# Performance work log

Hardware: AMD Instinct MI355X
Metric: run time of the kernel (lower is better)

Reference implementation:

```python
import jax, jax.numpy as jnp
import numpy as np

D_MODEL = 1024
NUM_HEADS = 16


def setup_inputs() -> dict:
    key = jax.random.key(0)
    ks = jax.random.split(key, 5)
    x = jax.random.normal(ks[0], (1, 4096, D_MODEL), dtype=jnp.float32)
    # Linear stores weight as [out_features, in_features]; init ~ trunc_normal, scaled for stability
    scale = 0.02
    wq = jax.random.normal(ks[1], (D_MODEL, D_MODEL), dtype=jnp.float32) * scale
    wk = jax.random.normal(ks[2], (D_MODEL, D_MODEL), dtype=jnp.float32) * scale
    wv = jax.random.normal(ks[3], (D_MODEL, D_MODEL), dtype=jnp.float32) * scale
    wo = jax.random.normal(ks[4], (D_MODEL, D_MODEL), dtype=jnp.float32) * scale
    return {"x": x, "wq": wq, "wk": wk, "wv": wv, "wo": wo}


def reference(x, wq, wk, wv, wo):
    # x: [B, S, D]; weights: [D, D] stored as [out, in] (y = x @ W.T)
    B, S, D = x.shape
    H = NUM_HEADS
    d_k = D // H
    q = x @ wq.T  # [B, S, D]
    k = x @ wk.T
    v = x @ wv.T
    # torch.split along last dim == reshape into contiguous head chunks
    qh = q.reshape(B, S, H, d_k).transpose(0, 2, 1, 3)  # [B, H, S, d_k]
    kh = k.reshape(B, S, H, d_k).transpose(0, 2, 1, 3)
    vh = v.reshape(B, S, H, d_k).transpose(0, 2, 1, 3)
    scores = jnp.einsum("bhqd,bhkd->bhqk", qh, kh) / jnp.sqrt(jnp.asarray(d_k, x.dtype))
    causal = jnp.tril(jnp.ones((S, S), dtype=bool))
    # original uses masked_fill(mask == 0, -10000.0), not -inf
    scores = jnp.where(causal, scores, jnp.asarray(-10000.0, x.dtype))
    attn = jax.nn.softmax(scores, axis=-1)  # stable (subtracts max), same math as module's Softmax
    ctx = jnp.einsum("bhqk,bhkd->bhqd", attn, vh)  # [B, H, S, d_k]
    ctx = ctx.transpose(0, 2, 1, 3).reshape(B, S, D)  # concat heads along last dim
    return ctx @ wo.T
```

## Files before the change

kernel.cpp:

```cpp
#include <hip/hip_runtime.h>
#include <stdint.h>

typedef short s16x8 __attribute__((ext_vector_type(8)));
typedef short s16x4 __attribute__((ext_vector_type(4)));
typedef float f32x4 __attribute__((ext_vector_type(4)));
typedef unsigned short u16;

#define S_LEN 4096
#define DM    1024
#define NH    16

__device__ __forceinline__ u16 f2bf(float f) {
  unsigned int u; __builtin_memcpy(&u, &f, 4);
  return (u16)((u + 0x7fffu + ((u >> 16) & 1u)) >> 16);
}

__device__ __forceinline__ void glds16(const void* gsrc, void* lds_uniform) {
  __builtin_amdgcn_global_load_lds(
      (const __attribute__((address_space(1))) unsigned int*)gsrc,
      (__attribute__((address_space(3))) unsigned int*)(unsigned int)(uintptr_t)lds_uniform,
      16, 0, 0);
}

__global__ __launch_bounds__(256)
void cast_all(const float* __restrict__ x,  const float* __restrict__ wq,
              const float* __restrict__ wk, const float* __restrict__ wv,
              const float* __restrict__ wo,
              u16* __restrict__ xb,  u16* __restrict__ wqb, u16* __restrict__ wkb,
              u16* __restrict__ wvb, u16* __restrict__ wob) {
  const int i = blockIdx.x * 256 + threadIdx.x;
  const float* src; u16* dst; int off;
  if (i < (1 << 20)) { src = x; dst = xb; off = i; }
  else {
    const int j = i - (1 << 20);
    const int seg = j >> 18;
    off = j & ((1 << 18) - 1);
    if (seg == 0)      { src = wq; dst = wqb; }
    else if (seg == 1) { src = wk; dst = wkb; }
    else if (seg == 2) { src = wv; dst = wvb; }
    else               { src = wo; dst = wob; }
  }
  float4 v = ((const float4*)src)[off];
  ushort4 o;
  o.x = f2bf(v.x); o.y = f2bf(v.y); o.z = f2bf(v.z); o.w = f2bf(v.w);
  ((ushort4*)dst)[off] = o;
}

#define GEMM_PROLOGUE()                                                        \
  __shared__ u16 SM[32768];                                                    \
  const int tid  = threadIdx.x;                                                \
  const int lane = tid & 63;                                                   \
  const int wave = tid >> 6;                                                   \
  const int g    = lane >> 4;                                                  \
  const int lr   = lane & 15;                                                  \
  const int x7   = lane & 7;                                                   \
  const int wr   = wave >> 1;                                                  \
  const int wc   = wave & 1;                                                   \
  const int a_base = wr * 8192 + lr * 128 + ((g ^ x7) << 4);                   \
  const int b_base = 0x8000 + wc * 8192 + lr * 128 + ((g ^ x7) << 4);          \
  const int stg_row = wave * 8 + (lane >> 3);                                  \
  const int gc      = (lane & 7) ^ (lane >> 3);                                \
  const int stg_dst = wave * 1024;                                             \
  const f32x4 zz = {0.f, 0.f, 0.f, 0.f};                                       \
  f32x4 acc[4][4];                                                             \
  _Pragma("unroll") for (int i = 0; i < 4; ++i)                                \
      _Pragma("unroll") for (int j = 0; j < 4; ++j) acc[i][j] = zz;

#define GEMM_KLOOP(Aptr, Wptr)                                                 \
  const u16* pa0 = Aptr + (size_t)(m0 +  0 + stg_row) * 1024 + gc * 8;         \
  const u16* pa1 = Aptr + (size_t)(m0 + 32 + stg_row) * 1024 + gc * 8;         \
  const u16* pa2 = Aptr + (size_t)(m0 + 64 + stg_row) * 1024 + gc * 8;         \
  const u16* pa3 = Aptr + (size_t)(m0 + 96 + stg_row) * 1024 + gc * 8;         \
  const u16* pw0 = Wptr + (size_t)(n0 +  0 + stg_row) * 1024 + gc * 8;         \
  const u16* pw1 = Wptr + (size_t)(n0 + 32 + stg_row) * 1024 + gc * 8;         \
  const u16* pw2 = Wptr + (size_t)(n0 + 64 + stg_row) * 1024 + gc * 8;         \
  const u16* pw3 = Wptr + (size_t)(n0 + 96 + stg_row) * 1024 + gc * 8;         \
  {                                                                            \
    glds16(pa0, (char*)SM + stg_dst);                                          \
    glds16(pa1, (char*)SM + 4096  + stg_dst);                                  \
    glds16(pa2, (char*)SM + 8192  + stg_dst);                                  \
    glds16(pa3, (char*)SM + 12288 + stg_dst);                                  \
    glds16(pw0, (char*)SM + 0x8000 + stg_dst);                                 \
    glds16(pw1, (char*)SM + 0x8000 + 4096  + stg_dst);                         \
    glds16(pw2, (char*)SM + 0x8000 + 8192  + stg_dst);                         \
    glds16(pw3, (char*)SM + 0x8000 + 12288 + stg_dst);                         \
  }                                                                            \
  int abuf = 0;                                                                \
  __syncthreads();                                                             \
  for (int kt = 0; kt < 16; ++kt) {                                            \
    if (kt + 1 < 16) {                                                         \
      pa0 += 64; pa1 += 64; pa2 += 64; pa3 += 64;                              \
      pw0 += 64; pw1 += 64; pw2 += 64; pw3 += 64;                              \
      const int nb = abuf ^ 0x4000;                                            \
      glds16(pa0, (char*)SM + nb + stg_dst);                                   \
      glds16(pa1, (char*)SM + nb + 4096  + stg_dst);                           \
      glds16(pa2, (char*)SM + nb + 8192  + stg_dst);                           \
      glds16(pa3, (char*)SM + nb + 12288 + stg_dst);                           \
      glds16(pw0, (char*)SM + 0x8000 + nb + stg_dst);                          \
      glds16(pw1, (char*)SM + 0x8000 + nb + 4096  + stg_dst);                  \
      glds16(pw2, (char*)SM + 0x8000 + nb + 8192  + stg_dst);                  \
      glds16(pw3, (char*)SM + 0x8000 + nb + 12288 + stg_dst);                  \
    }                                                                          \
    const int aoff = a_base + abuf;                                            \
    const int boff = b_base + abuf;                                            \
    _Pragma("unroll")                                                          \
    for (int kk = 0; kk < 2; ++kk) {                                           \
      const int ak = aoff ^ (kk << 6);                                         \
      const int bk = boff ^ (kk << 6);                                         \
      s16x8 af[4], bfr[4];                                                     \
      _Pragma("unroll") for (int mi = 0; mi < 4; ++mi)                         \
        af[mi] = *(const s16x8*)((const char*)SM + ak + mi * 2048);            \
      _Pragma("unroll") for (int nj = 0; nj < 4; ++nj)                         \
        bfr[nj] = *(const s16x8*)((const char*)SM + bk + nj * 2048);           \
      _Pragma("unroll") for (int mi = 0; mi < 4; ++mi)                         \
        _Pragma("unroll") for (int nj = 0; nj < 4; ++nj)                       \
          acc[mi][nj] = __builtin_amdgcn_mfma_f32_16x16x32_bf16(               \
              af[mi], bfr[nj], acc[mi][nj], 0, 0, 0);                          \
    }                                                                          \
    __syncthreads();                                                           \
    abuf ^= 0x4000;                                                            \
  }

__global__ __launch_bounds__(256)
void gemm_qkv(const u16* __restrict__ A, const u16* __restrict__ Wq,
              const u16* __restrict__ Wk, const u16* __restrict__ Wv,
              u16* __restrict__ Qo, u16* __restrict__ Ko, u16* __restrict__ VTo,
              float qscale) {
  const int m0 = blockIdx.y * 128;
  const int n0 = blockIdx.x * 128;
  const int z  = blockIdx.z;
  const u16* W = (z == 0) ? Wq : ((z == 1) ? Wk : Wv);
  GEMM_PROLOGUE();
  GEMM_KLOOP(A, W);

  const float scale = (z == 0) ? qscale : 1.0f;
  u16* outMK = (z == 0) ? Qo : Ko;
#pragma unroll
  for (int mi = 0; mi < 4; ++mi)
#pragma unroll
    for (int nj = 0; nj < 4; ++nj)
#pragma unroll
      for (int r = 0; r < 4; ++r) {
        const int m = m0 + wr * 64 + mi * 16 + g * 4 + r;
        const int n = n0 + wc * 64 + nj * 16 + lr;
        const u16 v = f2bf(acc[mi][nj][r] * scale);
        if (z < 2) outMK[(size_t)m * 1024 + n] = v;
        else {
          const int mp = (m & ~63) | (m & 0x23) | ((m & 0x0C) << 1) | ((m & 0x10) >> 2);
          VTo[(size_t)n * S_LEN + mp] = v;
        }
      }
}

__global__ __launch_bounds__(256)
void gemm_o(const u16* __restrict__ A, const u16* __restrict__ W, float* __restrict__ C) {
  const int m0 = blockIdx.y * 128;
  const int n0 = blockIdx.x * 128;
  GEMM_PROLOGUE();
  GEMM_KLOOP(A, W);

#pragma unroll
  for (int mi = 0; mi < 4; ++mi)
#pragma unroll
    for (int nj = 0; nj < 4; ++nj)
#pragma unroll
      for (int r = 0; r < 4; ++r) {
        const int m = m0 + wr * 64 + mi * 16 + g * 4 + r;
        const int n = n0 + wc * 64 + nj * 16 + lr;
        C[(size_t)m * 1024 + n] = acc[mi][nj][r];
      }
}

__global__ __launch_bounds__(256, 3)
void attn_kernel(const u16* __restrict__ Q, const u16* __restrict__ Kg,
                 const u16* __restrict__ VT, u16* __restrict__ Ctx) {
  __shared__ u16 SM[24576];
  const int tid  = threadIdx.x;
  const int lane = tid & 63;
  const int wave = tid >> 6;
  const int g    = lane >> 4;
  const int lr   = lane & 15;
  const int x7   = lane & 7;
  const int h  = blockIdx.x;
  const int qi = (int)gridDim.y - 1 - (int)blockIdx.y;
  const int q0 = qi * 64;
  const int wq0 = q0 + wave * 16;
  const int qg = wq0 + lr;
  const int nt = qi + 1;

  const int rd_base = lr * 128 + ((g ^ x7) << 4);

  const int stg_row = wave * 8 + (lane >> 3);
  const int gcs     = (lane & 7) ^ (lane >> 3);
  const int stg_dst = wave * 1024;
  const u16* kp0 = Kg + (size_t)(stg_row)      * DM + h * 64 + gcs * 8;
  const u16* kp1 = Kg + (size_t)(stg_row + 32) * DM + h * 64 + gcs * 8;
  const u16* vp0 = VT + (size_t)(h * 64 + stg_row)      * S_LEN + gcs * 8;
  const u16* vp1 = VT + (size_t)(h * 64 + stg_row + 32) * S_LEN + gcs * 8;

  s16x8 qf[2];
#pragma unroll
  for (int kk = 0; kk < 2; ++kk)
    qf[kk] = *(const s16x8*)(Q + (size_t)qg * DM + h * 64 + kk * 32 + g * 8);

  const f32x4 zz = {0.f, 0.f, 0.f, 0.f};
  f32x4 ctxa[4];
#pragma unroll
  for (int i = 0; i < 4; ++i) ctxa[i] = zz;
  float lsum = 0.f;

  auto STAGE = [&](int t, int ibuf) {
    const size_t koff = (size_t)t * 64 * DM;
    const int   voff  = t * 64;
    const int   kb    = ibuf << 13;
    glds16(kp0 + koff, (char*)SM + kb + stg_dst);
    glds16(kp1 + koff, (char*)SM + kb + 4096 + stg_dst);
    glds16(vp0 + voff, (char*)SM + 0x6000 + kb + stg_dst);
    glds16(vp1 + voff, (char*)SM + 0x6000 + kb + 4096 + stg_dst);
  };

  STAGE(0, 0);
  if (1 < nt) STAGE(1, 1);
  if (2 < nt) STAGE(2, 2);
  int ib = 0;

  for (int kt = 0; kt < nt; ++kt) {
    const int k0 = kt * 64;
    const int ahead = ((nt - 1 < kt + 2) ? nt - 1 : kt + 2) - kt;
    if (ahead == 2)      asm volatile("s_waitcnt vmcnt(8)" ::: "memory");
    else if (ahead == 1) asm volatile("s_waitcnt vmcnt(4)" ::: "memory");
    else                 asm volatile("s_waitcnt vmcnt(0)" ::: "memory");
    __builtin_amdgcn_sched_barrier(0);
    __builtin_amdgcn_s_barrier();
    __builtin_amdgcn_sched_barrier(0);

    const int kb = ib << 13;
    const bool active = (k0 <= wq0 + 15);
    if (active) {
      const int ka0 = rd_base + kb;
      f32x4 st[4];
#pragma unroll
      for (int f = 0; f < 4; ++f) st[f] = zz;
      __builtin_amdgcn_s_setprio(1);
#pragma unroll
      for (int kk = 0; kk < 2; ++kk) {
        const int ka = ka0 ^ (kk << 6);
#pragma unroll
        for (int f = 0; f < 4; ++f) {
          s16x8 kf = *(const s16x8*)((const char*)SM + ka + f * 2048);
          st[f] = __builtin_amdgcn_mfma_f32_16x16x32_bf16(kf, qf[kk], st[f], 0, 0, 0);
        }
      }
      __builtin_amdgcn_s_setprio(0);

      float ex[16];
      const bool anyMask = (k0 + 63 > wq0);
      if (anyMask) {
#pragma unroll
        for (int f = 0; f < 4; ++f)
#pragma unroll
          for (int r = 0; r < 4; ++r) {
            const int kpos = k0 + f * 16 + g * 4 + r;
            float e = exp2f(st[f][r]);
            ex[f * 4 + r] = (kpos > qg) ? 0.f : e;
          }
      } else {
#pragma unroll
        for (int f = 0; f < 4; ++f)
#pragma unroll
          for (int r = 0; r < 4; ++r)
            ex[f * 4 + r] = exp2f(st[f][r]);
      }
      float s4[4];
#pragma unroll
      for (int i = 0; i < 4; ++i)
        s4[i] = (ex[4 * i] + ex[4 * i + 1]) + (ex[4 * i + 2] + ex[4 * i + 3]);
      lsum += (s4[0] + s4[1]) + (s4[2] + s4[3]);

      union { s16x8 v; unsigned int u[4]; } P[2];
#pragma unroll
      for (int kh = 0; kh < 2; ++kh)
#pragma unroll
        for (int w = 0; w < 4; ++w)
          asm("v_cvt_pk_bf16_f32 %0, %1, %2"
              : "=v"(P[kh].u[w])
              : "v"(ex[kh * 8 + 2 * w]), "v"(ex[kh * 8 + 2 * w + 1]));

      const int va0 = rd_base + 0x6000 + kb;
      __builtin_amdgcn_s_setprio(1);
#pragma unroll
      for (int kh = 0; kh < 2; ++kh) {
        const int va = va0 ^ (kh << 6);
#pragma unroll
        for (int df = 0; df < 4; ++df) {
          s16x8 vf = *(const s16x8*)((const char*)SM + va + df * 2048);
          ctxa[df] = __builtin_amdgcn_mfma_f32_16x16x32_bf16(vf, P[kh].v, ctxa[df], 0, 0, 0);
        }
      }
      __builtin_amdgcn_s_setprio(0);
    }

    asm volatile("s_waitcnt lgkmcnt(0)" ::: "memory");
    __builtin_amdgcn_sched_barrier(0);
    __builtin_amdgcn_s_barrier();
    __builtin_amdgcn_sched_barrier(0);
    if (kt + 3 < nt) STAGE(kt + 3, ib);
    ib = (ib == 2) ? 0 : ib + 1;
  }

  float tot = lsum;
  tot += __shfl_xor(tot, 16);
  tot += __shfl_xor(tot, 32);
  const float inv = 1.0f / tot;
#pragma unroll
  for (int df = 0; df < 4; ++df)
#pragma unroll
    for (int r = 0; r < 4; ++r)
      Ctx[(size_t)qg * DM + h * 64 + df * 16 + g * 4 + r] = f2bf(ctxa[df][r] * inv);
}

extern "C" void kernel_launch(void* const* d_in, const int* in_sizes, int n_in,
                              void* d_out, int out_size, void* d_ws, size_t ws_size,
                              hipStream_t stream) {
  const float* x  = (const float*)d_in[0];
  const float* wq = (const float*)d_in[1];
  const float* wk = (const float*)d_in[2];
  const float* wv = (const float*)d_in[3];
  const float* wo = (const float*)d_in[4];

  u16* p = (u16*)d_ws;
  u16* xb  = p; p += (size_t)S_LEN * DM;
  u16* wqb = p; p += (size_t)DM * DM;
  u16* wkb = p; p += (size_t)DM * DM;
  u16* wvb = p; p += (size_t)DM * DM;
  u16* wob = p; p += (size_t)DM * DM;
  u16* Qb  = p; p += (size_t)S_LEN * DM;
  u16* Kb  = p; p += (size_t)S_LEN * DM;
  u16* VTb = p; p += (size_t)S_LEN * DM;
  u16* Cb  = p; p += (size_t)S_LEN * DM;
  if (ws_size < (size_t)(5 * S_LEN * DM + 4 * DM * DM) * 2) return;

  cast_all<<<dim3((2 * 1024 * 1024) / 256), 256, 0, stream>>>(
      x, wq, wk, wv, wo, xb, wqb, wkb, wvb, wob);

  const float QSCALE = 0.125f * 1.44269504088896f;
  gemm_qkv<<<dim3(DM / 128, S_LEN / 128, 3), 256, 0, stream>>>(
      xb, wqb, wkb, wvb, Qb, Kb, VTb, QSCALE);

  attn_kernel<<<dim3(NH, S_LEN / 64), 256, 0, stream>>>(Qb, Kb, VTb, Cb);

  gemm_o<<<dim3(DM / 128, S_LEN / 128), 256, 0, stream>>>(Cb, wob, (float*)d_out);
}
```

Measured before the change: 138.4 us.

## Switch attention to 32x32x16 MFMA with split-K waves and LDS reduction

Rewrites the attention inner loop to use 32x32x16 bf16 MFMAs. Waves are now arranged as a 2x2 grid of query halves by key halves, and the two key-half partial contexts and softmax sums are combined through LDS at the end. The V-transpose permutation in the QKV GEMM is changed to match the new MFMA operand layout, and exp2f is replaced with raw v_exp_f32. The goal is fewer MFMA issues and LDS reads per tile. In exchange it adds a final cross-wave reduction and sync, and the layout permutation must stay consistent with the new read pattern.

```diff
diff --git a/kernel.cpp b/kernel.cpp
--- a/kernel.cpp
+++ b/kernel.cpp
@@ -2,8 +2,8 @@
 #include <stdint.h>
 
 typedef short s16x8 __attribute__((ext_vector_type(8)));
-typedef short s16x4 __attribute__((ext_vector_type(4)));
 typedef float f32x4 __attribute__((ext_vector_type(4)));
+typedef float f32x16 __attribute__((ext_vector_type(16)));
 typedef unsigned short u16;
 
 #define S_LEN 4096
@@ -13,6 +13,12 @@
 __device__ __forceinline__ u16 f2bf(float f) {
   unsigned int u; __builtin_memcpy(&u, &f, 4);
   return (u16)((u + 0x7fffu + ((u >> 16) & 1u)) >> 16);
+}
+
+__device__ __forceinline__ float exp2_raw(float x) {
+  float r;
+  asm("v_exp_f32 %0, %1" : "=v"(r) : "v"(x));
+  return r;
 }
 
 __device__ __forceinline__ void glds16(const void* gsrc, void* lds_uniform) {
@@ -146,7 +152,7 @@
         const u16 v = f2bf(acc[mi][nj][r] * scale);
         if (z < 2) outMK[(size_t)m * 1024 + n] = v;
         else {
-          const int mp = (m & ~63) | (m & 0x23) | ((m & 0x0C) << 1) | ((m & 0x10) >> 2);
+          const int mp = (m & ~0x0C) | ((m & 0x04) << 1) | ((m & 0x08) >> 1);
           VTo[(size_t)n * S_LEN + mp] = v;
         }
       }
@@ -178,17 +184,18 @@
   const int tid  = threadIdx.x;
   const int lane = tid & 63;
   const int wave = tid >> 6;
-  const int g    = lane >> 4;
-  const int lr   = lane & 15;
+  const int qh   = wave >> 1;
+  const int kh   = wave & 1;
+  const int l31  = lane & 31;
+  const int hi   = lane >> 5;
   const int x7   = lane & 7;
   const int h  = blockIdx.x;
   const int qi = (int)gridDim.y - 1 - (int)blockIdx.y;
   const int q0 = qi * 64;
-  const int wq0 = q0 + wave * 16;
-  const int qg = wq0 + lr;
+  const int qg = q0 + 32 * qh + l31;
   const int nt = qi + 1;
 
-  const int rd_base = lr * 128 + ((g ^ x7) << 4);
+  const int k_base = (32 * kh + l31) * 128;
 
   const int stg_row = wave * 8 + (lane >> 3);
   const int gcs     = (lane & 7) ^ (lane >> 3);
@@ -198,15 +205,14 @@
   const u16* vp0 = VT + (size_t)(h * 64 + stg_row)      * S_LEN + gcs * 8;
   const u16* vp1 = VT + (size_t)(h * 64 + stg_row + 32) * S_LEN + gcs * 8;
 
-  s16x8 qf[2];
-#pragma unroll
-  for (int kk = 0; kk < 2; ++kk)
-    qf[kk] = *(const s16x8*)(Q + (size_t)qg * DM + h * 64 + kk * 32 + g * 8);
-
-  const f32x4 zz = {0.f, 0.f, 0.f, 0.f};
-  f32x4 ctxa[4];
-#pragma unroll
-  for (int i = 0; i < 4; ++i) ctxa[i] = zz;
+  s16x8 qf[4];
+#pragma unroll
+  for (int s = 0; s < 4; ++s)
+    qf[s] = *(const s16x8*)(Q + (size_t)qg * DM + h * 64 + 16 * s + 8 * hi);
+
+  f32x16 ctx0 = {0,0,0,0,0,0,0,0,0,0,0,0,0,0,0,0};
+  f32x16 ctx1 = ctx0;
+  const f32x16 zz16 = ctx0;
   float lsum = 0.f;
 
   auto STAGE = [&](int t, int ibuf) {
@@ -235,41 +241,31 @@
     __builtin_amdgcn_sched_barrier(0);
 
     const int kb = ib << 13;
-    const bool active = (k0 <= wq0 + 15);
+    const int kbase_abs = k0 + 32 * kh;
+    const bool active = (kbase_abs <= q0 + 32 * qh + 31);
     if (active) {
-      const int ka0 = rd_base + kb;
-      f32x4 st[4];
-#pragma unroll
-      for (int f = 0; f < 4; ++f) st[f] = zz;
+      f32x16 st = zz16;
       __builtin_amdgcn_s_setprio(1);
 #pragma unroll
-      for (int kk = 0; kk < 2; ++kk) {
-        const int ka = ka0 ^ (kk << 6);
-#pragma unroll
-        for (int f = 0; f < 4; ++f) {
-          s16x8 kf = *(const s16x8*)((const char*)SM + ka + f * 2048);
-          st[f] = __builtin_amdgcn_mfma_f32_16x16x32_bf16(kf, qf[kk], st[f], 0, 0, 0);
+      for (int s = 0; s < 4; ++s) {
+        s16x8 kf = *(const s16x8*)((const char*)SM + kb + k_base +
+                                   (((2 * s + hi) ^ x7) << 4));
+        st = __builtin_amdgcn_mfma_f32_32x32x16_bf16(kf, qf[s], st, 0, 0, 0);
+      }
+      __builtin_amdgcn_s_setprio(0);
+
+      float ex[16];
+      const bool anyMask = (kbase_abs + 31 > q0 + 32 * qh);
+      if (anyMask) {
+#pragma unroll
+        for (int r = 0; r < 16; ++r) {
+          const int kpos = kbase_abs + (r & 3) + 8 * (r >> 2) + 4 * hi;
+          float e = exp2_raw(st[r]);
+          ex[r] = (kpos > qg) ? 0.f : e;
         }
-      }
-      __builtin_amdgcn_s_setprio(0);
-
-      float ex[16];
-      const bool anyMask = (k0 + 63 > wq0);
-      if (anyMask) {
-#pragma unroll
-        for (int f = 0; f < 4; ++f)
-#pragma unroll
-          for (int r = 0; r < 4; ++r) {
-            const int kpos = k0 + f * 16 + g * 4 + r;
-            float e = exp2f(st[f][r]);
-            ex[f * 4 + r] = (kpos > qg) ? 0.f : e;
-          }
       } else {
 #pragma unroll
-        for (int f = 0; f < 4; ++f)
-#pragma unroll
-          for (int r = 0; r < 4; ++r)
-            ex[f * 4 + r] = exp2f(st[f][r]);
+        for (int r = 0; r < 16; ++r) ex[r] = exp2_raw(st[r]);
       }
       float s4[4];
 #pragma unroll
@@ -277,25 +273,23 @@
         s4[i] = (ex[4 * i] + ex[4 * i + 1]) + (ex[4 * i + 2] + ex[4 * i + 3]);
       lsum += (s4[0] + s4[1]) + (s4[2] + s4[3]);
 
-      union { s16x8 v; unsigned int u[4]; } P[2];
-#pragma unroll
-      for (int kh = 0; kh < 2; ++kh)
+      union Pu { s16x8 v; unsigned int u[4]; } P[2];
+#pragma unroll
+      for (int s = 0; s < 2; ++s)
 #pragma unroll
         for (int w = 0; w < 4; ++w)
           asm("v_cvt_pk_bf16_f32 %0, %1, %2"
-              : "=v"(P[kh].u[w])
-              : "v"(ex[kh * 8 + 2 * w]), "v"(ex[kh * 8 + 2 * w + 1]));
-
-      const int va0 = rd_base + 0x6000 + kb;
+              : "=v"(P[s].u[w])
+              : "v"(ex[s * 8 + 2 * w]), "v"(ex[s * 8 + 2 * w + 1]));
+
       __builtin_amdgcn_s_setprio(1);
 #pragma unroll
-      for (int kh = 0; kh < 2; ++kh) {
-        const int va = va0 ^ (kh << 6);
-#pragma unroll
-        for (int df = 0; df < 4; ++df) {
-          s16x8 vf = *(const s16x8*)((const char*)SM + va + df * 2048);
-          ctxa[df] = __builtin_amdgcn_mfma_f32_16x16x32_bf16(vf, P[kh].v, ctxa[df], 0, 0, 0);
-        }
+      for (int s = 0; s < 2; ++s) {
+        const int ch = ((4 * kh + 2 * s + hi) ^ x7) << 4;
+        s16x8 v0 = *(const s16x8*)((const char*)SM + 0x6000 + kb + l31 * 128 + ch);
+        ctx0 = __builtin_amdgcn_mfma_f32_32x32x16_bf16(v0, P[s].v, ctx0, 0, 0, 0);
+        s16x8 v1 = *(const s16x8*)((const char*)SM + 0x6000 + kb + (32 + l31) * 128 + ch);
+        ctx1 = __builtin_amdgcn_mfma_f32_32x32x16_bf16(v1, P[s].v, ctx1, 0, 0, 0);
       }
       __builtin_amdgcn_s_setprio(0);
     }
@@ -308,15 +302,31 @@
     ib = (ib == 2) ? 0 : ib + 1;
   }
 
-  float tot = lsum;
-  tot += __shfl_xor(tot, 16);
-  tot += __shfl_xor(tot, 32);
-  const float inv = 1.0f / tot;
-#pragma unroll
-  for (int df = 0; df < 4; ++df)
-#pragma unroll
-    for (int r = 0; r < 4; ++r)
-      Ctx[(size_t)qg * DM + h * 64 + df * 16 + g * 4 + r] = f2bf(ctxa[df][r] * inv);
+  lsum += __shfl_xor(lsum, 32);
+  const int pbase = qh * 0x2800;
+  if (kh == 1) {
+#pragma unroll
+    for (int r = 0; r < 16; ++r) {
+      const int drow = (r & 3) + 8 * (r >> 2) + 4 * hi;
+      *(float*)((char*)SM + pbase + ((drow)      * 32 + l31) * 4) = ctx0[r];
+      *(float*)((char*)SM + pbase + ((32 + drow) * 32 + l31) * 4) = ctx1[r];
+    }
+    if (lane < 32) *(float*)((char*)SM + pbase + 0x2000 + l31 * 4) = lsum;
+  }
+  __syncthreads();
+  if (kh == 0) {
+    const float ls1 = *(const float*)((const char*)SM + pbase + 0x2000 + l31 * 4);
+    const float inv = 1.0f / (lsum + ls1);
+    u16* outp = Ctx + (size_t)qg * DM + h * 64;
+#pragma unroll
+    for (int r = 0; r < 16; ++r) {
+      const int drow = (r & 3) + 8 * (r >> 2) + 4 * hi;
+      const float c0 = ctx0[r] + *(const float*)((const char*)SM + pbase + ((drow) * 32 + l31) * 4);
+      const float c1 = ctx1[r] + *(const float*)((const char*)SM + pbase + ((32 + drow) * 32 + l31) * 4);
+      outp[drow]      = f2bf(c0 * inv);
+      outp[32 + drow] = f2bf(c1 * inv);
+    }
+  }
 }
 
 extern "C" void kernel_launch(void* const* d_in, const int* in_sizes, int n_in,
```

Result: faster. 126.0 us (-8.9%).
